# Kernel optimization log

Hardware: AMD Instinct MI355X
Metric: run time of the kernel (lower is better)

Reference implementation:

```python
import math
import jax, jax.numpy as jnp
import numpy as np

B, C, F_, W = 4, 2, 512, 1024
NH = 8
HD = F_ // NH            # 64 head dim
ROT = HD // 2            # 32 rotated dims
NFREQ = ROT // 2         # 16 base freqs ('pixel': linspace(1, max_freq/2, dim//2)*pi)


def mc_linear(x, w_pw):
    # x: [b,c,f_in,w], w_pw: [c, f_out, f_in] -> [b,c,f_out,w]
    return jnp.einsum('bchw,cgh->bcgw', x, w_pw)


def apply_rope(t, freqs):
    # t: [b,c,n,w,d]; freqs: [w, rot_dim] (already pair-repeated)
    rot_dim = freqs.shape[-1]
    t_rot, t_pass = t[..., :rot_dim], t[..., rot_dim:]
    cos, sin = jnp.cos(freqs), jnp.sin(freqs)
    x1, x2 = t_rot[..., 0::2], t_rot[..., 1::2]
    rh = jnp.stack([-x2, x1], axis=-1).reshape(t_rot.shape)  # rotate_half (interleaved pairs)
    return jnp.concatenate([t_rot * cos + rh * sin, t_pass], axis=-1)


def setup_inputs() -> dict:
    key = jax.random.key(0)
    ks = jax.random.split(key, 6)
    x = jax.random.normal(ks[0], (B, C, F_, W), dtype=jnp.float32)
    bound = 1.0 / math.sqrt(F_)
    def w(k):
        return jax.random.uniform(k, (C, F_, F_), minval=-bound, maxval=bound, dtype=jnp.float32)
    wq, wk, wv, wo = w(ks[1]), w(ks[2]), w(ks[3]), w(ks[4])
    # learned 'pixel' freqs: linspace(1., max_freq/2=5., NFREQ) * pi
    freqs_param = (jnp.linspace(1.0, 5.0, NFREQ) * math.pi).astype(jnp.float32)
    return {"x": x, "wq": wq, "wk": wk, "wv": wv, "wo": wo, "freqs_param": freqs_param}


def reference(x, wq, wk, wv, wo, freqs_param):
    b, c, h, w = x.shape
    def heads(t):  # [b,c,h,w] -> [b,c,NH,w,HD]
        return t.transpose(0, 1, 3, 2).reshape(b, c, w, NH, HD).transpose(0, 1, 3, 2, 4)
    pos = jnp.arange(w, dtype=jnp.float32)
    freqs = jnp.repeat(pos[:, None] * freqs_param[None, :], 2, axis=-1)  # [w, ROT]
    # NOTE: original module uses q_proj for q, k, and v (k_proj/v_proj unused)
    q = apply_rope(heads(mc_linear(x, wq)), freqs)
    k = apply_rope(heads(mc_linear(x, wq)), freqs)
    v = heads(mc_linear(x, wq))
    qk = jnp.einsum('bcnqd,bcnkd->bcnqk', q, k) / math.sqrt(h)
    a = jnp.einsum('bcnqk,bcnkd->bcnqd', jax.nn.softmax(qk, axis=-1), v)
    a = a.transpose(0, 1, 3, 2, 4).reshape(b, c, w, NH * HD).transpose(0, 1, 3, 2)  # [b,c,h,w]
    return mc_linear(a, wo)
```

## Files before the change

kernel.cpp:

```cpp
#include <hip/hip_runtime.h>
#include <hip/hip_bf16.h>
#include <math.h>

#define B_ 4
#define C_ 2
#define F_ 512
#define W_ 1024
#define NH_ 8
#define HD_ 64
#define ROT_ 32
#define NFREQ_ 16
#define BC_ (B_*C_)

#define QSC_ 0.2525048f

typedef short bf16x8 __attribute__((ext_vector_type(8)));
typedef float f32x4  __attribute__((ext_vector_type(4)));
typedef float f32x16 __attribute__((ext_vector_type(16)));
typedef unsigned short u16;
typedef unsigned int   u32;

#if __has_builtin(__builtin_amdgcn_exp2f)
#define EXP2(x) __builtin_amdgcn_exp2f(x)
#else
#define EXP2(x) exp2f(x)
#endif

#define VDRAIN() asm volatile("s_waitcnt vmcnt(0)" ::: "memory")

__device__ __forceinline__ u16 f2bf(float f) {
    union { float f; u32 u; } v; v.f = f;
    u32 r = (v.u + 0x7fffu + ((v.u >> 16) & 1u)) >> 16;
    return (u16)r;
}
__device__ __forceinline__ float bf2f(u16 h) {
    union { u32 u; float f; } v; v.u = ((u32)h) << 16;
    return v.f;
}
__device__ __forceinline__ f32x4 mfma16(bf16x8 a, bf16x8 b, f32x4 c) {
    return __builtin_amdgcn_mfma_f32_16x16x32_bf16(a, b, c, 0, 0, 0);
}
__device__ __forceinline__ f32x16 mfma32(bf16x8 a, bf16x8 b, f32x16 c) {
    return __builtin_amdgcn_mfma_f32_32x32x16_bf16(a, b, c, 0, 0, 0);
}
__device__ __forceinline__ void gload16(const u16* g, u16* l) {
    __builtin_amdgcn_global_load_lds(
        (const __attribute__((address_space(1))) u32*)g,
        (__attribute__((address_space(3))) u32*)l, 16, 0, 0);
}
__device__ __forceinline__ u32 pk2(float lo, float hi) {
    __hip_bfloat162 h = __float22bfloat162_rn(make_float2(lo, hi));
    union { __hip_bfloat162 b; u32 u; } cv; cv.b = h; return cv.u;
}
__device__ __forceinline__ void pl32swap(u32& a, u32& b) {
    asm volatile("v_permlane32_swap_b32 %0, %1" : "+v"(a), "+v"(b));
}

__global__ __launch_bounds__(256)
void prep_all(const float* __restrict__ wq, const float* __restrict__ wo,
              const float* __restrict__ fp, const float* __restrict__ x,
              u16* __restrict__ wqh, u16* __restrict__ woh, u16* __restrict__ wol,
              float2* __restrict__ trig, u16* __restrict__ xh)
{
    __shared__ float T[64][65];
    const int b = blockIdx.x, t = threadIdx.x;
    if (b < 512) {
        int i = (b * 256 + t) * 4;
        float4 v = *(const float4*)(wq + i);
        ushort4 h;
        h.x = f2bf(v.x); h.y = f2bf(v.y); h.z = f2bf(v.z); h.w = f2bf(v.w);
        *(ushort4*)(wqh + i) = h;
    } else if (b < 1024) {
        int i = ((b - 512) * 256 + t) * 4;
        float4 v = *(const float4*)(wo + i);
        ushort4 h, l;
        h.x = f2bf(v.x); l.x = f2bf(v.x - bf2f(h.x));
        h.y = f2bf(v.y); l.y = f2bf(v.y - bf2f(h.y));
        h.z = f2bf(v.z); l.z = f2bf(v.z - bf2f(h.z));
        h.w = f2bf(v.w); l.w = f2bf(v.w - bf2f(h.w));
        *(ushort4*)(woh + i) = h;
        *(ushort4*)(wol + i) = l;
    } else if (b < 1088) {
        int idx = (b - 1024) * 256 + t;
        int w = idx >> 4, j = idx & 15;
        float th = (float)w * fp[j];
        float s, c;
        sincosf(th, &s, &c);
        trig[idx] = make_float2(c, s);
    } else {
        const int b2 = b - 1088;
        const int h0 = (b2 & 7) * 64, w0 = ((b2 >> 3) & 15) * 64, bc = b2 >> 7;
        {
            const int hl = t >> 2, wc = (t & 3) * 16;
            const float* src = x + ((size_t)bc * F_ + h0 + hl) * W_ + w0 + wc;
            #pragma unroll
            for (int z = 0; z < 4; ++z)
                *(float4*)(&T[hl][wc + z * 4]) = *(const float4*)(src + z * 4);
        }
        __syncthreads();
        {
            const int wl = t >> 2, hc = (t & 3) * 16;
            u16 hv[16];
            #pragma unroll
            for (int z = 0; z < 16; ++z) hv[z] = f2bf(T[hc + z][wl]);
            size_t base = ((size_t)bc * W_ + w0 + wl) * F_ + h0 + hc;
            *(uint4*)(xh + base)     = *(uint4*)(hv);
            *(uint4*)(xh + base + 8) = *(uint4*)(hv + 8);
        }
    }
}

template<int MODE>
__global__ __launch_bounds__(256)
void gemm4(const u16* __restrict__ Ah_, const u16* __restrict__ Al_,
           const u16* __restrict__ Bh_,
           u16* __restrict__ Vout, u16* __restrict__ Qout,
           float* __restrict__ Fout, const float2* __restrict__ trig)
{
    constexpr int BUFS  = MODE ? 8192 : 6144;
    constexpr int B_OFF = MODE ? 4096 : 2048;
    __shared__ u16 sh[2 * BUFS];

    const int tid = threadIdx.x, lane = tid & 63, wid = tid >> 6;
    const int wm = wid >> 1, wn = wid & 1;
    const int m0 = blockIdx.x * 64, n0 = blockIdx.y * 128, bc = blockIdx.z, c = bc % C_;
    const u16* Abh = Ah_ + (size_t)c * F_ * F_;
    const u16* Abl = MODE ? (Al_ + (size_t)c * F_ * F_) : (const u16*)nullptr;
    const u16* Bbh = Bh_ + (size_t)bc * W_ * F_;

    f32x4 acc[2][4] = {};
    const int srow = tid >> 2, sslot = tid & 3;

    auto STAGE = [&](int k0, int buf) {
        u16* base = sh + buf * BUFS;
        {
            const int ts = sslot ^ ((srow >> 1) & 3);
            const size_t ga = (size_t)(m0 + srow) * F_ + k0 + ts * 8;
            gload16(Abh + ga, base + wid * 512);
            if constexpr (MODE) gload16(Abl + ga, base + 2048 + wid * 512);
        }
        #pragma unroll
        for (int h = 0; h < 2; ++h) {
            const int brow = h * 64 + srow;
            const int ts = sslot ^ ((brow >> 1) & 3);
            const size_t gb = (size_t)(n0 + brow) * F_ + k0 + ts * 8;
            gload16(Bbh + gb, base + B_OFF + h * 2048 + wid * 512);
        }
    };

    STAGE(0, 0);
    VDRAIN();
    __syncthreads();
    int cur = 0;
    for (int kt = 0; kt < 16; ++kt) {
        if (kt < 15) STAGE((kt + 1) * 32, cur ^ 1);
        const u16* Ash = sh + cur * BUFS;
        const u16* Asl = Ash + 2048;
        const u16* Bsh = Ash + B_OFF;

        bf16x8 fah[2], fal[2];
        #pragma unroll
        for (int i = 0; i < 2; ++i) {
            const int row = wm * 32 + i * 16 + (lane & 15);
            const int idx = row * 32 + (((lane >> 4) ^ ((row >> 1) & 3)) << 3);
            fah[i] = *(const bf16x8*)(&Ash[idx]);
            if constexpr (MODE) fal[i] = *(const bf16x8*)(&Asl[idx]);
        }
        #pragma unroll
        for (int j = 0; j < 4; ++j) {
            const int rowb = wn * 64 + j * 16 + (lane & 15);
            const int idxb = rowb * 32 + (((lane >> 4) ^ ((rowb >> 1) & 3)) << 3);
            bf16x8 bh = *(const bf16x8*)(&Bsh[idxb]);
            #pragma unroll
            for (int i = 0; i < 2; ++i)
                acc[i][j] = mfma16(fah[i], bh, acc[i][j]);
            if constexpr (MODE) {
                #pragma unroll
                for (int i = 0; i < 2; ++i)
                    acc[i][j] = mfma16(fal[i], bh, acc[i][j]);
            }
        }
        VDRAIN();
        __syncthreads();
        cur ^= 1;
    }

    #pragma unroll
    for (int i = 0; i < 2; ++i) {
        const int gr = m0 + wm * 32 + i * 16 + (lane >> 4) * 4;
        #pragma unroll
        for (int j = 0; j < 4; ++j) {
            const int wc = n0 + wn * 64 + j * 16 + (lane & 15);
            #pragma unroll
            for (int r = 0; r < 4; ++r) {
                const size_t ad = ((size_t)bc * F_ + gr + r) * W_ + wc;
                if constexpr (MODE == 1) Fout[ad] = acc[i][j][r];
                else                     Vout[ad] = f2bf(acc[i][j][r]);
            }
        }
    }

    if constexpr (MODE == 0) {
        __syncthreads();
        u16* Qt = sh + wid * 2048;
        const int head = blockIdx.x;
        #pragma unroll
        for (int j = 0; j < 4; ++j) {
            const int wl = j * 16 + (lane & 15);
            const int wg = n0 + wn * 64 + wl;
            #pragma unroll
            for (int i = 0; i < 2; ++i) {
                float q[4];
                if (wm == 0) {
                    #pragma unroll
                    for (int p = 0; p < 2; ++p) {
                        const int fidx = i * 8 + (lane >> 4) * 2 + p;
                        float2 cs = trig[wg * NFREQ_ + fidx];
                        float e = acc[i][j][2 * p], o = acc[i][j][2 * p + 1];
                        q[2 * p]     = (e * cs.x - o * cs.y) * QSC_;
                        q[2 * p + 1] = (o * cs.x + e * cs.y) * QSC_;
                    }
                } else {
                    #pragma unroll
                    for (int r = 0; r < 4; ++r) q[r] = acc[i][j][r] * QSC_;
                }
                #pragma unroll
                for (int r = 0; r < 4; ++r) {
                    const int ddl = i * 16 + (lane >> 4) * 4 + r;
                    Qt[wl * 32 + ((ddl & 7) | (((ddl >> 3) ^ (wl & 3)) << 3))] = f2bf(q[r]);
                }
            }
        }
        const size_t qrow = (((size_t)bc * NH_ + head) * W_ + n0 + wn * 64 + lane) * 64 + wm * 32;
        #pragma unroll
        for (int s = 0; s < 4; ++s) {
            uint4 v = *(const uint4*)(&Qt[lane * 32 + ((s ^ (lane & 3)) << 3)]);
            *(uint4*)(&Qout[qrow + s * 8]) = v;
        }
    }
}

__global__ __launch_bounds__(128)
void attn4(const u16* __restrict__ Qt, const u16* __restrict__ Vg,
           u16* __restrict__ AhO)
{
    __shared__ u16 sh[8192];
    const int tid = threadIdx.x, lane = tid & 63, wid = tid >> 6;
    const int q0 = blockIdx.x * 64, head = blockIdx.y, bc = blockIdx.z;
    const u16* qb = Qt + ((size_t)bc * NH_ + head) * W_ * 64;
    const u16* vb = Vg + ((size_t)bc * F_ + head * HD_) * W_;

    const int qcol = lane & 31, hi = lane >> 5;
    const int srow = lane >> 3, st = lane & 7;

    bf16x8 qf[4];
    {
        const u16* qrow = qb + (size_t)(q0 + wid * 32 + qcol) * 64 + hi * 8;
        #pragma unroll
        for (int ks = 0; ks < 4; ++ks)
            qf[ks] = *(const bf16x8*)(qrow + ks * 16);
    }

    f32x16 o0, o1;
    #pragma unroll
    for (int i = 0; i < 16; ++i) { o0[i] = 0.f; o1[i] = 0.f; }
    float lsum = 0.f;

    auto STAGE = [&](int kt, int buf) {
        const int k0 = kt * 64;
        u16* Vsb = sh + buf * 4096;
        #pragma unroll
        for (int p = 0; p < 4; ++p) {
            const int rb = wid * 32 + p * 8;
            const int r  = rb + srow;
            const int ts = st ^ (r & 7);
            gload16(vb + (size_t)r * W_ + k0 + ts * 8, Vsb + rb * 64);
        }
    };

    STAGE(0, 0);
    VDRAIN();
    __syncthreads();
    int cur = 0;
    for (int kt = 0; kt < 16; ++kt) {
        if (kt < 15) STAGE(kt + 1, cur ^ 1);
        const u16* Vs = sh + cur * 4096;
        const int k0 = kt * 64;

        f32x16 s0, s1;
        #pragma unroll
        for (int i = 0; i < 16; ++i) { s0[i] = 0.f; s1[i] = 0.f; }
        #pragma unroll
        for (int ks = 0; ks < 4; ++ks) {
            const int sl = ks * 2 + hi;
            bf16x8 kf0 = *(const bf16x8*)(qb + (size_t)(k0 + qcol) * 64 + sl * 8);
            bf16x8 kf1 = *(const bf16x8*)(qb + (size_t)(k0 + 32 + qcol) * 64 + sl * 8);
            s0 = mfma32(kf0, qf[ks], s0);
            s1 = mfma32(kf1, qf[ks], s1);
        }

        float p0[16], p1[16];
        #pragma unroll
        for (int i = 0; i < 16; ++i) { p0[i] = EXP2(s0[i]); p1[i] = EXP2(s1[i]); }
        float part = 0.f;
        #pragma unroll
        for (int i = 0; i < 16; ++i) part += p0[i] + p1[i];
        lsum += part;

        bf16x8 pf[4];
        #pragma unroll
        for (int kb = 0; kb < 2; ++kb) {
            const float* pp = kb ? p1 : p0;
            #pragma unroll
            for (int f = 0; f < 2; ++f) {
                u32 a1 = pk2(pp[f*8+0], pp[f*8+1]);
                u32 a2 = pk2(pp[f*8+2], pp[f*8+3]);
                u32 b1 = pk2(pp[f*8+4], pp[f*8+5]);
                u32 b2 = pk2(pp[f*8+6], pp[f*8+7]);
                pl32swap(a1, b1);
                pl32swap(a2, b2);
                union { u32 w[4]; bf16x8 v; } u;
                u.w[0] = a1; u.w[1] = a2; u.w[2] = b1; u.w[3] = b2;
                pf[kb * 2 + f] = u.v;
            }
        }

        #pragma unroll
        for (int ks2 = 0; ks2 < 4; ++ks2) {
            const int sl = ks2 * 2 + hi;
            const int d0r = qcol;
            const int d1r = 32 + qcol;
            bf16x8 vf0 = *(const bf16x8*)(Vs + d0r * 64 + ((sl ^ (d0r & 7)) << 3));
            bf16x8 vf1 = *(const bf16x8*)(Vs + d1r * 64 + ((sl ^ (d1r & 7)) << 3));
            o0 = mfma32(vf0, pf[ks2], o0);
            o1 = mfma32(vf1, pf[ks2], o1);
        }
        VDRAIN();
        __syncthreads();
        cur ^= 1;
    }

    lsum += __shfl_xor(lsum, 32);
    const float inv = 1.f / lsum;

    const int wrow = q0 + wid * 32 + qcol;
    const size_t rowbase = ((size_t)bc * W_ + wrow) * F_ + head * HD_;
    #pragma unroll
    for (int dblk = 0; dblk < 2; ++dblk) {
        const f32x16 ov = dblk ? o1 : o0;
        const int coloff = dblk * 32;
        #pragma unroll
        for (int pr = 0; pr < 8; ++pr) {
            const float v1 = ov[2 * pr]     * inv;
            const float v2 = ov[2 * pr + 1] * inv;
            const int drow = ((2 * pr) & 3) + 8 * (pr >> 1) + 4 * hi;
            const u16 h1 = f2bf(v1), h2 = f2bf(v2);
            *(u32*)(AhO + rowbase + coloff + drow) = (u32)h1 | ((u32)h2 << 16);
        }
    }
}

extern "C" void kernel_launch(void* const* d_in, const int* in_sizes, int n_in,
                              void* d_out, int out_size, void* d_ws, size_t ws_size,
                              hipStream_t stream) {
    const float* x  = (const float*)d_in[0];
    const float* wq = (const float*)d_in[1];
    const float* wo = (const float*)d_in[4];
    const float* fp = (const float*)d_in[5];
    float* out = (float*)d_out;

    char* w8 = (char*)d_ws;
    const size_t MB = 1024 * 1024;
    u16* xh   = (u16*)(w8);
    u16* wqh  = (u16*)(w8 + 8 * MB);
    u16* woh  = (u16*)(w8 + 9 * MB);
    u16* wol  = (u16*)(w8 + 10 * MB);
    float2* trig = (float2*)(w8 + 11 * MB);
    u16* qbuf = (u16*)(w8 + 12 * MB);
    u16* vbuf = (u16*)(w8 + 20 * MB);
    u16* ah   = xh;

    prep_all<<<2112, 256, 0, stream>>>(wq, wo, fp, x, wqh, woh, wol, trig, xh);

    gemm4<0><<<dim3(8, 8, 8), 256, 0, stream>>>(
        wqh, nullptr, xh, vbuf, qbuf, nullptr, trig);

    attn4<<<dim3(16, NH_, BC_), 128, 0, stream>>>(qbuf, vbuf, ah);

    gemm4<1><<<dim3(8, 8, 8), 256, 0, stream>>>(
        woh, wol, ah, nullptr, nullptr, out, trig);
}
```

Baseline: 163.4 us.

## Double query rows per attention block and stage K tiles in LDS

The attention kernel now gives each wave 64 query rows instead of 32, so every K and V fragment read is reused across two query sub-tiles. K tiles are now staged asynchronously into shared memory alongside V, with swizzling, instead of being read straight from global memory in the inner loop. The grid is halved to 512 blocks and LDS use doubles, which raises register pressure (four f32x16 accumulators plus four score tiles) and may cut occupancy and parallelism.

```diff
diff --git a/kernel.cpp b/kernel.cpp
--- a/kernel.cpp
+++ b/kernel.cpp
@@ -241,40 +241,45 @@
 }
 
 __global__ __launch_bounds__(128)
-void attn4(const u16* __restrict__ Qt, const u16* __restrict__ Vg,
+void attn5(const u16* __restrict__ Qt, const u16* __restrict__ Vg,
            u16* __restrict__ AhO)
 {
-    __shared__ u16 sh[8192];
+    __shared__ u16 sh[16384];
     const int tid = threadIdx.x, lane = tid & 63, wid = tid >> 6;
-    const int q0 = blockIdx.x * 64, head = blockIdx.y, bc = blockIdx.z;
+    const int q0 = blockIdx.x * 128, head = blockIdx.y, bc = blockIdx.z;
     const u16* qb = Qt + ((size_t)bc * NH_ + head) * W_ * 64;
     const u16* vb = Vg + ((size_t)bc * F_ + head * HD_) * W_;
 
     const int qcol = lane & 31, hi = lane >> 5;
     const int srow = lane >> 3, st = lane & 7;
 
-    bf16x8 qf[4];
+    bf16x8 qfA[4], qfB[4];
     {
-        const u16* qrow = qb + (size_t)(q0 + wid * 32 + qcol) * 64 + hi * 8;
-        #pragma unroll
-        for (int ks = 0; ks < 4; ++ks)
-            qf[ks] = *(const bf16x8*)(qrow + ks * 16);
-    }
-
-    f32x16 o0, o1;
+        const u16* qra = qb + (size_t)(q0 + wid * 64 + qcol) * 64 + hi * 8;
+        const u16* qrb = qra + 32 * 64;
+        #pragma unroll
+        for (int ks = 0; ks < 4; ++ks) {
+            qfA[ks] = *(const bf16x8*)(qra + ks * 16);
+            qfB[ks] = *(const bf16x8*)(qrb + ks * 16);
+        }
+    }
+
+    f32x16 oA0, oA1, oB0, oB1;
     #pragma unroll
-    for (int i = 0; i < 16; ++i) { o0[i] = 0.f; o1[i] = 0.f; }
-    float lsum = 0.f;
+    for (int i = 0; i < 16; ++i) { oA0[i]=0.f; oA1[i]=0.f; oB0[i]=0.f; oB1[i]=0.f; }
+    float lsumA = 0.f, lsumB = 0.f;
 
     auto STAGE = [&](int kt, int buf) {
         const int k0 = kt * 64;
-        u16* Vsb = sh + buf * 4096;
+        u16* Ksb = sh + buf * 8192;
+        u16* Vsb = Ksb + 4096;
         #pragma unroll
         for (int p = 0; p < 4; ++p) {
             const int rb = wid * 32 + p * 8;
             const int r  = rb + srow;
             const int ts = st ^ (r & 7);
-            gload16(vb + (size_t)r * W_ + k0 + ts * 8, Vsb + rb * 64);
+            gload16(qb + (size_t)(k0 + r) * 64 + ts * 8, Ksb + rb * 64);
+            gload16(vb + (size_t)r * W_ + k0 + ts * 8,   Vsb + rb * 64);
         }
     };
 
@@ -284,33 +289,36 @@
     int cur = 0;
     for (int kt = 0; kt < 16; ++kt) {
         if (kt < 15) STAGE(kt + 1, cur ^ 1);
-        const u16* Vs = sh + cur * 4096;
-        const int k0 = kt * 64;
-
-        f32x16 s0, s1;
-        #pragma unroll
-        for (int i = 0; i < 16; ++i) { s0[i] = 0.f; s1[i] = 0.f; }
+        const u16* Ks = sh + cur * 8192;
+        const u16* Vs = Ks + 4096;
+
+        f32x16 sA0, sA1, sB0, sB1;
+        #pragma unroll
+        for (int i = 0; i < 16; ++i) { sA0[i]=0.f; sA1[i]=0.f; sB0[i]=0.f; sB1[i]=0.f; }
         #pragma unroll
         for (int ks = 0; ks < 4; ++ks) {
             const int sl = ks * 2 + hi;
-            bf16x8 kf0 = *(const bf16x8*)(qb + (size_t)(k0 + qcol) * 64 + sl * 8);
-            bf16x8 kf1 = *(const bf16x8*)(qb + (size_t)(k0 + 32 + qcol) * 64 + sl * 8);
-            s0 = mfma32(kf0, qf[ks], s0);
-            s1 = mfma32(kf1, qf[ks], s1);
-        }
-
-        float p0[16], p1[16];
-        #pragma unroll
-        for (int i = 0; i < 16; ++i) { p0[i] = EXP2(s0[i]); p1[i] = EXP2(s1[i]); }
-        float part = 0.f;
-        #pragma unroll
-        for (int i = 0; i < 16; ++i) part += p0[i] + p1[i];
-        lsum += part;
-
-        bf16x8 pf[4];
-        #pragma unroll
-        for (int kb = 0; kb < 2; ++kb) {
-            const float* pp = kb ? p1 : p0;
+            const int kA = qcol, kB = 32 + qcol;
+            bf16x8 kf0 = *(const bf16x8*)(Ks + kA * 64 + ((sl ^ (kA & 7)) << 3));
+            bf16x8 kf1 = *(const bf16x8*)(Ks + kB * 64 + ((sl ^ (kB & 7)) << 3));
+            sA0 = mfma32(kf0, qfA[ks], sA0);
+            sA1 = mfma32(kf1, qfA[ks], sA1);
+            sB0 = mfma32(kf0, qfB[ks], sB0);
+            sB1 = mfma32(kf1, qfB[ks], sB1);
+        }
+
+        #pragma unroll
+        for (int i = 0; i < 16; ++i) {
+            sA0[i] = EXP2(sA0[i]); sA1[i] = EXP2(sA1[i]);
+            sB0[i] = EXP2(sB0[i]); sB1[i] = EXP2(sB1[i]);
+        }
+        float pa = 0.f, pb = 0.f;
+        #pragma unroll
+        for (int i = 0; i < 16; ++i) { pa += sA0[i] + sA1[i]; pb += sB0[i] + sB1[i]; }
+        lsumA += pa; lsumB += pb;
+
+        bf16x8 pfA[4], pfB[4];
+        auto PACK = [&](const f32x16& pp, bf16x8* dst) {
             #pragma unroll
             for (int f = 0; f < 2; ++f) {
                 u32 a1 = pk2(pp[f*8+0], pp[f*8+1]);
@@ -321,41 +329,49 @@
                 pl32swap(a2, b2);
                 union { u32 w[4]; bf16x8 v; } u;
                 u.w[0] = a1; u.w[1] = a2; u.w[2] = b1; u.w[3] = b2;
-                pf[kb * 2 + f] = u.v;
+                dst[f] = u.v;
             }
-        }
+        };
+        PACK(sA0, pfA); PACK(sA1, pfA + 2);
+        PACK(sB0, pfB); PACK(sB1, pfB + 2);
 
         #pragma unroll
         for (int ks2 = 0; ks2 < 4; ++ks2) {
             const int sl = ks2 * 2 + hi;
-            const int d0r = qcol;
-            const int d1r = 32 + qcol;
+            const int d0r = qcol, d1r = 32 + qcol;
             bf16x8 vf0 = *(const bf16x8*)(Vs + d0r * 64 + ((sl ^ (d0r & 7)) << 3));
             bf16x8 vf1 = *(const bf16x8*)(Vs + d1r * 64 + ((sl ^ (d1r & 7)) << 3));
-            o0 = mfma32(vf0, pf[ks2], o0);
-            o1 = mfma32(vf1, pf[ks2], o1);
+            oA0 = mfma32(vf0, pfA[ks2], oA0);
+            oA1 = mfma32(vf1, pfA[ks2], oA1);
+            oB0 = mfma32(vf0, pfB[ks2], oB0);
+            oB1 = mfma32(vf1, pfB[ks2], oB1);
         }
         VDRAIN();
         __syncthreads();
         cur ^= 1;
     }
 
-    lsum += __shfl_xor(lsum, 32);
-    const float inv = 1.f / lsum;
-
-    const int wrow = q0 + wid * 32 + qcol;
-    const size_t rowbase = ((size_t)bc * W_ + wrow) * F_ + head * HD_;
+    lsumA += __shfl_xor(lsumA, 32);
+    lsumB += __shfl_xor(lsumB, 32);
+    const float invA = 1.f / lsumA, invB = 1.f / lsumB;
+
     #pragma unroll
-    for (int dblk = 0; dblk < 2; ++dblk) {
-        const f32x16 ov = dblk ? o1 : o0;
-        const int coloff = dblk * 32;
-        #pragma unroll
-        for (int pr = 0; pr < 8; ++pr) {
-            const float v1 = ov[2 * pr]     * inv;
-            const float v2 = ov[2 * pr + 1] * inv;
-            const int drow = ((2 * pr) & 3) + 8 * (pr >> 1) + 4 * hi;
-            const u16 h1 = f2bf(v1), h2 = f2bf(v2);
-            *(u32*)(AhO + rowbase + coloff + drow) = (u32)h1 | ((u32)h2 << 16);
+    for (int qs = 0; qs < 2; ++qs) {
+        const float inv = qs ? invB : invA;
+        const int wrow = q0 + wid * 64 + qs * 32 + qcol;
+        const size_t rowbase = ((size_t)bc * W_ + wrow) * F_ + head * HD_;
+        #pragma unroll
+        for (int dblk = 0; dblk < 2; ++dblk) {
+            const f32x16 ov = qs ? (dblk ? oB1 : oB0) : (dblk ? oA1 : oA0);
+            const int coloff = dblk * 32;
+            #pragma unroll
+            for (int pr = 0; pr < 8; ++pr) {
+                const float v1 = ov[2 * pr]     * inv;
+                const float v2 = ov[2 * pr + 1] * inv;
+                const int drow = ((2 * pr) & 3) + 8 * (pr >> 1) + 4 * hi;
+                const u16 h1 = f2bf(v1), h2 = f2bf(v2);
+                *(u32*)(AhO + rowbase + coloff + drow) = (u32)h1 | ((u32)h2 << 16);
+            }
         }
     }
 }
@@ -385,7 +401,7 @@
     gemm4<0><<<dim3(8, 8, 8), 256, 0, stream>>>(
         wqh, nullptr, xh, vbuf, qbuf, nullptr, trig);
 
-    attn4<<<dim3(16, NH_, BC_), 128, 0, stream>>>(qbuf, vbuf, ah);
+    attn5<<<dim3(8, NH_, BC_), 128, 0, stream>>>(qbuf, vbuf, ah);
 
     gemm4<1><<<dim3(8, 8, 8), 256, 0, stream>>>(
         woh, wol, ah, nullptr, nullptr, out, trig);
```

After: 143.8 us. 12.0% less time.
